# Kernel tuning notes

Hardware: AMD Instinct MI355X
Metric: run time of the kernel (lower is better)

## Reference

```python
import math
import jax, jax.numpy as jnp
import numpy as np

LOW_FREQ = 1
FACTOR = 1


def setup_inputs() -> dict:
    key = jax.random.key(0)
    x = jax.random.normal(key, (8, 4096, 512), dtype=jnp.float32)
    return {"x": x}


def reference(x):
    b, t, d = x.shape
    x_freq = jnp.fft.rfft(x, axis=1)  # (b, t//2+1, d) complex
    if t % 2 == 0:
        x_freq = x_freq[:, LOW_FREQ:-1]
        f = jnp.fft.rfftfreq(t)[LOW_FREQ:-1]
    else:
        x_freq = x_freq[:, LOW_FREQ:]
        f = jnp.fft.rfftfreq(t)[LOW_FREQ:]
    length = x_freq.shape[1]
    top_k = int(FACTOR * math.log(length))

    # top-k |X(f)| independently per (batch, channel)
    amp_all = jnp.abs(x_freq)                      # (b, F, d)
    _, idx = jax.lax.top_k(jnp.transpose(amp_all, (0, 2, 1)), top_k)  # (b, d, k)
    idx = jnp.transpose(idx, (0, 2, 1))            # (b, k, d)
    x_sel = jnp.take_along_axis(x_freq, idx, axis=1)  # (b, k, d) complex
    f_sel = f[idx].astype(jnp.float32)             # (b, k, d)

    # extrapolate: append conjugate components with negated frequency
    x2 = jnp.concatenate([x_sel, jnp.conj(x_sel)], axis=1)  # (b, 2k, d)
    f2 = jnp.concatenate([f_sel, -f_sel], axis=1)           # (b, 2k, d)
    amp = jnp.abs(x2)[:, :, None, :]               # (b, 2k, 1, d)
    phase = jnp.angle(x2)[:, :, None, :]           # (b, 2k, 1, d)
    tt = jnp.arange(t, dtype=jnp.float32)[None, None, :, None]  # (1,1,t,1)
    x_time = amp * jnp.cos(2.0 * math.pi * f2[:, :, None, :] * tt + phase)  # (b,2k,t,d)
    return jnp.sum(x_time, axis=1)                 # (b, t, d)
```

## Files before the change

kernel.cpp:

```cpp
#include <hip/hip_runtime.h>
#include <math.h>

#define B 8
#define T 4096
#define D 512
#define NPAIR ((B * D) / 2)
#define TOPK 7
#define LOG2T 12
#define PAD(e) ((e) + ((e) >> 4))
#define ZSZ (T + (T >> 4))

__device__ __forceinline__ int brev12(int x) {
  return (int)(__brev((unsigned)x) >> (32 - LOG2T));
}

__global__ __launch_bounds__(256) void k_transpose_pack(const float* __restrict__ x,
                                                        float2* __restrict__ xp) {
  __shared__ float tT[64][65];
  const int b  = blockIdx.z;
  const int t0 = blockIdx.x * 64;
  const int d0 = blockIdx.y * 64;
  const int tid = threadIdx.x;

  const int c4 = tid & 15;
  const int r0 = tid >> 4;
  for (int r = r0; r < 64; r += 16) {
    const float4 v = *(const float4*)&x[((size_t)b * T + (t0 + r)) * D + d0 + 4 * c4];
    tT[4 * c4 + 0][r] = v.x;
    tT[4 * c4 + 1][r] = v.y;
    tT[4 * c4 + 2][r] = v.z;
    tT[4 * c4 + 3][r] = v.w;
  }
  __syncthreads();

  const int tt  = tid & 31;
  const int rp0 = tid >> 5;
  for (int rp = rp0; rp < 32; rp += 8) {
    const float2 a  = *(const float2*)&tT[2 * rp][2 * tt];
    const float2 bb = *(const float2*)&tT[2 * rp + 1][2 * tt];
    const float4 o = make_float4(a.x, bb.x, a.y, bb.y);
    *(float4*)&xp[((size_t)b * (D / 2) + (d0 / 2 + rp)) * T + t0 + 2 * tt] = o;
  }
}

__global__ __launch_bounds__(256) void k_fft_topk(float2* __restrict__ xp) {
  __shared__ float2 Z[ZSZ];
  __shared__ float  s_rv[4];
  __shared__ int    s_rk[4];
  __shared__ float4 s_cf[2 * TOPK];

  const int tid = threadIdx.x;
  float2* g = xp + (size_t)blockIdx.x * T;

  for (int t = tid; t < T; t += 256) Z[PAD(t)] = g[t];
  __syncthreads();

  for (int s = 0; s < 6; ++s) {
    const int shift = 10 - 2 * s;
    const int q = 1 << shift;
    const float ang_scale = -6.283185307179586f / (float)(q << 2);
    for (int i = tid; i < T / 4; i += 256) {
      const int p    = i & (q - 1);
      const int base = ((i >> shift) << (shift + 2)) | p;
      float2 a0 = Z[PAD(base)];
      float2 a1 = Z[PAD(base + q)];
      float2 a2 = Z[PAD(base + 2 * q)];
      float2 a3 = Z[PAD(base + 3 * q)];
      float sw, cw;
      __sincosf(ang_scale * (float)p, &sw, &cw);
      const float c2 = cw * cw - sw * sw, s2 = 2.0f * cw * sw;
      const float c3 = c2 * cw - s2 * sw, s3 = c2 * sw + s2 * cw;
      const float t0r = a0.x + a2.x, t0i = a0.y + a2.y;
      const float t1r = a0.x - a2.x, t1i = a0.y - a2.y;
      const float t2r = a1.x + a3.x, t2i = a1.y + a3.y;
      const float t3r = a1.x - a3.x, t3i = a1.y - a3.y;
      Z[PAD(base)] = make_float2(t0r + t2r, t0i + t2i);
      const float u1r = t0r - t2r, u1i = t0i - t2i;
      Z[PAD(base + q)] = make_float2(u1r * c2 - u1i * s2, u1r * s2 + u1i * c2);
      const float u2r = t1r + t3i, u2i = t1i - t3r;
      Z[PAD(base + 2 * q)] = make_float2(u2r * cw - u2i * sw, u2r * sw + u2i * cw);
      const float u3r = t1r - t3i, u3i = t1i + t3r;
      Z[PAD(base + 3 * q)] = make_float2(u3r * c3 - u3i * s3, u3r * s3 + u3i * c3);
    }
    __syncthreads();
  }

  float a1v[8], a2v[8];
  #pragma unroll
  for (int j = 0; j < 8; ++j) {
    const int k = 1 + tid + (j << 8);
    if (k >= T / 2) { a1v[j] = -1e30f; a2v[j] = -1e30f; continue; }
    const float2 zk = Z[PAD(brev12(k))];
    const float2 zn = Z[PAD(brev12(T - k))];
    const float x1r = 0.5f * (zk.x + zn.x), x1i = 0.5f * (zk.y - zn.y);
    const float x2r = 0.5f * (zk.y + zn.y), x2i = 0.5f * (zn.x - zk.x);
    a1v[j] = x1r * x1r + x1i * x1i;
    a2v[j] = x2r * x2r + x2i * x2i;
  }

  for (int sh = 0; sh < 2; ++sh) {
    for (int it = 0; it < TOPK; ++it) {
      float bv = -1e30f;
      int bj = 0;
      #pragma unroll
      for (int j = 0; j < 8; ++j) {
        const float v = (sh == 0) ? a1v[j] : a2v[j];
        if (v > bv) { bv = v; bj = j; }
      }
      int bk = 1 + tid + (bj << 8);
      #pragma unroll
      for (int off = 1; off < 64; off <<= 1) {
        const float ov = __shfl_xor(bv, off);
        const int   ok = __shfl_xor(bk, off);
        if (ov > bv) { bv = ov; bk = ok; }
      }
      if ((tid & 63) == 0) { s_rv[tid >> 6] = bv; s_rk[tid >> 6] = bk; }
      __syncthreads();
      float wv = s_rv[0];
      int   wk = s_rk[0];
      #pragma unroll
      for (int w = 1; w < 4; ++w)
        if (s_rv[w] > wv) { wv = s_rv[w]; wk = s_rk[w]; }
      if (((wk - 1) & 255) == tid) {
        const int j = (wk - 1) >> 8;
        #pragma unroll
        for (int jj = 0; jj < 8; ++jj)
          if (jj == j) { if (sh == 0) a1v[jj] = -1e30f; else a2v[jj] = -1e30f; }
      }
      if (tid == 0) {
        const float2 zk = Z[PAD(brev12(wk))];
        const float2 zn = Z[PAD(brev12(T - wk))];
        float re, im;
        if (sh == 0) { re = 0.5f * (zk.x + zn.x); im = 0.5f * (zk.y - zn.y); }
        else         { re = 0.5f * (zk.y + zn.y); im = 0.5f * (zn.x - zk.x); }
        s_cf[sh * TOPK + it] = make_float4((float)wk, re, im, 0.0f);
      }
      __syncthreads();
    }
  }

  float4* cf = (float4*)g;
  if (tid < 2 * TOPK) cf[tid] = s_cf[tid];
}

__global__ __launch_bounds__(256) void k_eval(const float* __restrict__ ws,
                                              float* __restrict__ out) {
  __shared__ float  tile[64][64];
  __shared__ float4 s_coef[64 * TOPK];

  const int tid = threadIdx.x;
  const int b   = blockIdx.z;
  const int d0  = blockIdx.y * 64;
  const int t0  = blockIdx.x * 64;

  for (int idx = tid; idx < 64 * TOPK; idx += 256) {
    const int s = idx / TOPK, j = idx - s * TOPK;
    const int P = (b * D + d0) / 2 + (s >> 1);
    const int sh = s & 1;
    s_coef[idx] = ((const float4*)(ws + (size_t)P * (2 * T)))[sh * TOPK + j];
  }
  __syncthreads();

  const int dl = tid & 63;
  const int tg = tid >> 6;
  const float w0 = 6.283185307179586f / 4096.0f;

  float re[TOPK], im[TOPK], cc[TOPK], ss[TOPK], cd[TOPK], sd[TOPK];
  const int ts = t0 + tg;
  #pragma unroll
  for (int j = 0; j < TOPK; ++j) {
    const float4 v = s_coef[dl * TOPK + j];
    const int k = (int)v.x;
    re[j] = 2.0f * v.y;
    im[j] = 2.0f * v.z;
    const float a0 = w0 * (float)((k * ts) & (T - 1));
    const float ad = w0 * (float)((4 * k) & (T - 1));
    ss[j] = __sinf(a0); cc[j] = __cosf(a0);
    sd[j] = __sinf(ad); cd[j] = __cosf(ad);
  }

  #pragma unroll
  for (int i = 0; i < 16; ++i) {
    float acc = 0.0f;
    #pragma unroll
    for (int j = 0; j < TOPK; ++j) {
      acc += re[j] * cc[j] - im[j] * ss[j];
      const float nc = cc[j] * cd[j] - ss[j] * sd[j];
      const float ns = ss[j] * cd[j] + cc[j] * sd[j];
      cc[j] = nc; ss[j] = ns;
    }
    tile[tg + 4 * i][dl] = acc;
  }
  __syncthreads();

  const int c4 = tid & 15;
  const int rw = tid >> 4;
  for (int rr = rw; rr < 64; rr += 16) {
    const float4 v = *(const float4*)&tile[rr][4 * c4];
    *(float4*)&out[((size_t)b * T + (t0 + rr)) * D + d0 + 4 * c4] = v;
  }
}

extern "C" void kernel_launch(void* const* d_in, const int* in_sizes, int n_in,
                              void* d_out, int out_size, void* d_ws, size_t ws_size,
                              hipStream_t stream) {
  const float* x = (const float*)d_in[0];
  float* out = (float*)d_out;
  float2* xp = (float2*)d_ws;

  dim3 tgrid(T / 64, D / 64, B);
  hipLaunchKernelGGL(k_transpose_pack, tgrid, dim3(256), 0, stream, x, xp);
  hipLaunchKernelGGL(k_fft_topk, dim3(NPAIR), dim3(256), 0, stream, xp);
  hipLaunchKernelGGL(k_eval, tgrid, dim3(256), 0, stream, (const float*)d_ws, out);
}
```

Measured before the change: 201.1 us.

## Replace radix-4 shared-memory FFT with register radix-16 three-pass FFT

Replaces the six-stage radix-4 FFT, which makes a shared-memory pass and a barrier per stage, with a three-pass 16x16x16 decomposition. Each pass does a register-resident 16-point DFT with constant twiddles, and the first pass loads directly from global memory. Digit-reversed indexing replaces bit reversal. The top-k loop now double-buffers its reduction scratch so one barrier per iteration can be dropped, and it adds index tie-breaking. This cuts shared-memory traffic, sincos calls and barriers, at the cost of higher register pressure from the 16-element arrays.

```diff
diff --git a/kernel.cpp b/kernel.cpp
--- a/kernel.cpp
+++ b/kernel.cpp
@@ -6,13 +6,56 @@
 #define D 512
 #define NPAIR ((B * D) / 2)
 #define TOPK 7
-#define LOG2T 12
 #define PAD(e) ((e) + ((e) >> 4))
-#define ZSZ (T + (T >> 4))
-
-__device__ __forceinline__ int brev12(int x) {
-  return (int)(__brev((unsigned)x) >> (32 - LOG2T));
-}
+
+__device__ __forceinline__ int drev(int k) {
+  return ((k & 15) << 8) | (k & 240) | (k >> 8);
+}
+
+__device__ __forceinline__ float2 cmul(float2 a, float2 b) {
+  return make_float2(a.x * b.x - a.y * b.y, a.x * b.y + a.y * b.x);
+}
+__device__ __forceinline__ float2 cadd(float2 a, float2 b) { return make_float2(a.x + b.x, a.y + b.y); }
+__device__ __forceinline__ float2 csub(float2 a, float2 b) { return make_float2(a.x - b.x, a.y - b.y); }
+__device__ __forceinline__ float2 cmul_negi(float2 a) { return make_float2(a.y, -a.x); }
+
+__device__ __forceinline__ void dft4(float2& a, float2& b, float2& c, float2& d) {
+  const float2 t0 = cadd(a, c), t1 = csub(a, c);
+  const float2 t2 = cadd(b, d), t3n = cmul_negi(csub(b, d));
+  a = cadd(t0, t2);
+  b = cadd(t1, t3n);
+  c = csub(t0, t2);
+  d = csub(t1, t3n);
+}
+
+#define C16 0.92387953251f
+#define S16 0.38268343236f
+#define RS2 0.70710678119f
+__device__ __forceinline__ void dft16(float2 r[16]) {
+  dft4(r[0], r[4], r[8],  r[12]);
+  dft4(r[1], r[5], r[9],  r[13]);
+  dft4(r[2], r[6], r[10], r[14]);
+  dft4(r[3], r[7], r[11], r[15]);
+  const float2 W1 = make_float2(C16, -S16);
+  const float2 W2 = make_float2(RS2, -RS2);
+  const float2 W3 = make_float2(S16, -C16);
+  const float2 W6 = make_float2(-RS2, -RS2);
+  const float2 W9 = make_float2(-C16, S16);
+  r[5]  = cmul(r[5],  W1);
+  r[9]  = cmul(r[9],  W2);
+  r[13] = cmul(r[13], W3);
+  r[6]  = cmul(r[6],  W2);
+  r[10] = cmul_negi(r[10]);
+  r[14] = cmul(r[14], W6);
+  r[7]  = cmul(r[7],  W3);
+  r[11] = cmul(r[11], W6);
+  r[15] = cmul(r[15], W9);
+  dft4(r[0],  r[1],  r[2],  r[3]);
+  dft4(r[4],  r[5],  r[6],  r[7]);
+  dft4(r[8],  r[9],  r[10], r[11]);
+  dft4(r[12], r[13], r[14], r[15]);
+}
+#define SW4(k) ((((k) & 3) << 2) | ((k) >> 2))
 
 __global__ __launch_bounds__(256) void k_transpose_pack(const float* __restrict__ x,
                                                         float2* __restrict__ xp) {
@@ -44,54 +87,69 @@
 }
 
 __global__ __launch_bounds__(256) void k_fft_topk(float2* __restrict__ xp) {
-  __shared__ float2 Z[ZSZ];
-  __shared__ float  s_rv[4];
-  __shared__ int    s_rk[4];
+  __shared__ float2 Z[PAD(T - 1) + 1];
+  __shared__ float  s_rv[2][4];
+  __shared__ int    s_rk[2][4];
   __shared__ float4 s_cf[2 * TOPK];
 
   const int tid = threadIdx.x;
   float2* g = xp + (size_t)blockIdx.x * T;
 
-  for (int t = tid; t < T; t += 256) Z[PAD(t)] = g[t];
-  __syncthreads();
-
-  for (int s = 0; s < 6; ++s) {
-    const int shift = 10 - 2 * s;
-    const int q = 1 << shift;
-    const float ang_scale = -6.283185307179586f / (float)(q << 2);
-    for (int i = tid; i < T / 4; i += 256) {
-      const int p    = i & (q - 1);
-      const int base = ((i >> shift) << (shift + 2)) | p;
-      float2 a0 = Z[PAD(base)];
-      float2 a1 = Z[PAD(base + q)];
-      float2 a2 = Z[PAD(base + 2 * q)];
-      float2 a3 = Z[PAD(base + 3 * q)];
-      float sw, cw;
-      __sincosf(ang_scale * (float)p, &sw, &cw);
-      const float c2 = cw * cw - sw * sw, s2 = 2.0f * cw * sw;
-      const float c3 = c2 * cw - s2 * sw, s3 = c2 * sw + s2 * cw;
-      const float t0r = a0.x + a2.x, t0i = a0.y + a2.y;
-      const float t1r = a0.x - a2.x, t1i = a0.y - a2.y;
-      const float t2r = a1.x + a3.x, t2i = a1.y + a3.y;
-      const float t3r = a1.x - a3.x, t3i = a1.y - a3.y;
-      Z[PAD(base)] = make_float2(t0r + t2r, t0i + t2i);
-      const float u1r = t0r - t2r, u1i = t0i - t2i;
-      Z[PAD(base + q)] = make_float2(u1r * c2 - u1i * s2, u1r * s2 + u1i * c2);
-      const float u2r = t1r + t3i, u2i = t1i - t3r;
-      Z[PAD(base + 2 * q)] = make_float2(u2r * cw - u2i * sw, u2r * sw + u2i * cw);
-      const float u3r = t1r - t3i, u3i = t1i + t3r;
-      Z[PAD(base + 3 * q)] = make_float2(u3r * c3 - u3i * s3, u3r * s3 + u3i * c3);
-    }
-    __syncthreads();
-  }
+  float2 r[16];
+  #pragma unroll
+  for (int a = 0; a < 16; ++a) r[a] = g[(a << 8) + tid];
+
+  dft16(r);
+  {
+    float s, c;
+    __sincosf(6.283185307179586f / 4096.0f * (float)tid, &s, &c);
+    const float2 w = make_float2(c, -s);
+    float2 t = make_float2(1.0f, 0.0f);
+    Z[PAD(tid)] = r[0];
+    #pragma unroll
+    for (int k1 = 1; k1 < 16; ++k1) {
+      t = cmul(t, w);
+      Z[PAD((k1 << 8) + tid)] = cmul(r[SW4(k1)], t);
+    }
+  }
+  __syncthreads();
+
+  {
+    const int m1 = tid & 15;
+    const int base = ((tid >> 4) << 8) + m1;
+    #pragma unroll
+    for (int m2 = 0; m2 < 16; ++m2) r[m2] = Z[PAD(base + (m2 << 4))];
+    dft16(r);
+    float s, c;
+    __sincosf(6.283185307179586f / 256.0f * (float)m1, &s, &c);
+    const float2 w = make_float2(c, -s);
+    float2 t = make_float2(1.0f, 0.0f);
+    Z[PAD(base)] = r[0];
+    #pragma unroll
+    for (int p = 1; p < 16; ++p) {
+      t = cmul(t, w);
+      Z[PAD(base + (p << 4))] = cmul(r[SW4(p)], t);
+    }
+  }
+  __syncthreads();
+
+  {
+    const int base = tid << 4;
+    #pragma unroll
+    for (int m1 = 0; m1 < 16; ++m1) r[m1] = Z[PAD(base + m1)];
+    dft16(r);
+    #pragma unroll
+    for (int q = 0; q < 16; ++q) Z[PAD(base + q)] = r[SW4(q)];
+  }
+  __syncthreads();
 
   float a1v[8], a2v[8];
   #pragma unroll
   for (int j = 0; j < 8; ++j) {
     const int k = 1 + tid + (j << 8);
     if (k >= T / 2) { a1v[j] = -1e30f; a2v[j] = -1e30f; continue; }
-    const float2 zk = Z[PAD(brev12(k))];
-    const float2 zn = Z[PAD(brev12(T - k))];
+    const float2 zk = Z[PAD(drev(k))];
+    const float2 zn = Z[PAD(drev(T - k))];
     const float x1r = 0.5f * (zk.x + zn.x), x1i = 0.5f * (zk.y - zn.y);
     const float x2r = 0.5f * (zk.y + zn.y), x2i = 0.5f * (zn.x - zk.x);
     a1v[j] = x1r * x1r + x1i * x1i;
@@ -100,6 +158,7 @@
 
   for (int sh = 0; sh < 2; ++sh) {
     for (int it = 0; it < TOPK; ++it) {
+      const int buf = (sh * TOPK + it) & 1;
       float bv = -1e30f;
       int bj = 0;
       #pragma unroll
@@ -112,15 +171,18 @@
       for (int off = 1; off < 64; off <<= 1) {
         const float ov = __shfl_xor(bv, off);
         const int   ok = __shfl_xor(bk, off);
-        if (ov > bv) { bv = ov; bk = ok; }
-      }
-      if ((tid & 63) == 0) { s_rv[tid >> 6] = bv; s_rk[tid >> 6] = bk; }
+        if (ov > bv || (ov == bv && ok < bk)) { bv = ov; bk = ok; }
+      }
+      if ((tid & 63) == 0) { s_rv[buf][tid >> 6] = bv; s_rk[buf][tid >> 6] = bk; }
       __syncthreads();
-      float wv = s_rv[0];
-      int   wk = s_rk[0];
+      float wv = s_rv[buf][0];
+      int   wk = s_rk[buf][0];
       #pragma unroll
-      for (int w = 1; w < 4; ++w)
-        if (s_rv[w] > wv) { wv = s_rv[w]; wk = s_rk[w]; }
+      for (int w = 1; w < 4; ++w) {
+        const float ov = s_rv[buf][w];
+        const int   ok = s_rk[buf][w];
+        if (ov > wv || (ov == wv && ok < wk)) { wv = ov; wk = ok; }
+      }
       if (((wk - 1) & 255) == tid) {
         const int j = (wk - 1) >> 8;
         #pragma unroll
@@ -128,16 +190,16 @@
           if (jj == j) { if (sh == 0) a1v[jj] = -1e30f; else a2v[jj] = -1e30f; }
       }
       if (tid == 0) {
-        const float2 zk = Z[PAD(brev12(wk))];
-        const float2 zn = Z[PAD(brev12(T - wk))];
+        const float2 zk = Z[PAD(drev(wk))];
+        const float2 zn = Z[PAD(drev(T - wk))];
         float re, im;
         if (sh == 0) { re = 0.5f * (zk.x + zn.x); im = 0.5f * (zk.y - zn.y); }
         else         { re = 0.5f * (zk.y + zn.y); im = 0.5f * (zn.x - zk.x); }
         s_cf[sh * TOPK + it] = make_float4((float)wk, re, im, 0.0f);
       }
-      __syncthreads();
-    }
-  }
+    }
+  }
+  __syncthreads();
 
   float4* cf = (float4*)g;
   if (tid < 2 * TOPK) cf[tid] = s_cf[tid];
```

New measurement: 199.5 us. No clear change (-0.8%).
